# Optimization experiments

Measured on AMD Instinct MI355X. Metric: run time of the kernel, lower is better.

## Reference

```python
import jax, jax.numpy as jnp
import numpy as np


def setup_inputs() -> dict:
    key = jax.random.key(0)
    k1, k2, k3 = jax.random.split(key, 3)
    N, C, H, W, S = 9, 32, 192, 256, 9  # 1 ref + 8 src views, 3x3 patch samples
    f = jax.random.normal(k1, (N, C, H, W, S), dtype=jnp.float32)
    Wp = jax.random.normal(k2, (C, C), dtype=jnp.float32) / np.sqrt(C)  # Conv1d(C,C,1) weight
    bp = jax.random.normal(k3, (C,), dtype=jnp.float32) * 0.01  # Conv1d bias
    return {"f": f, "Wp": Wp, "bp": bp, "o": 2, "G": 8}


def reference(f, Wp, bp, o, G):
    # f: (N, C, H, W, S); view 0 is the reference image, views 1..N-1 are sources.
    N, C, H, W, S = f.shape
    ref = f[0]          # (C, H, W, S)
    src = f[1:]         # (N-1, C, H, W, S)

    # 1x1 Conv1d projection of the reference patches (per-position linear).
    proj = jnp.einsum('dc,chws->dhws', Wp, ref) + bp[:, None, None, None]  # (C,H,W,S)

    # Dot-product attention of the center sample (S//2) against all S samples.
    logits = jnp.sum(proj[:, :, :, S // 2, None] * proj, axis=0) / jnp.sqrt(jnp.float32(C))  # (H,W,S)
    att = jax.nn.softmax(logits, axis=-1)  # (H,W,S)

    # Grouped correlation: split channels into G groups of Cg, dot within each group.
    Cg = C // G
    ref_g = ref.reshape(G, Cg, H, W, S)
    src_g = src.reshape(N - 1, G, Cg, H, W, S)
    gc = jnp.einsum('gchws,ngchws->nghws', ref_g, src_g)  # (N-1, G, H, W, S)

    # Attention-weighted reduction over the S patch-sample axis.
    return jnp.sum(gc * att[None, None], axis=-1)  # (N-1, G, H, W)
```

## Files before the change

### kernel.cpp

```cpp
#include <hip/hip_runtime.h>
#include <math.h>

#define NSRC 8
#define CCH  32
#define HH   192
#define WW   256
#define SS   9
#define GG   8

#define F_SC (HH*WW*SS)
#define F_SH (WW*SS)
#define F_SN (CCH*HH*WW*SS)

#define WS_M   0
#define WS_V   1024
#define WS_BB  1056

__global__ void k0_precompute(const float* __restrict__ Wp,
                              const float* __restrict__ bp,
                              float* __restrict__ ws) {
    const float inv_sqrtC = 0.17677669529663687f;
    int t = threadIdx.x;
    for (int idx = t; idx < 1024; idx += 256) {
        int c = idx >> 5, c2 = idx & 31;
        float acc = 0.f;
        for (int d = 0; d < 32; ++d) acc = fmaf(Wp[d*32 + c], Wp[d*32 + c2], acc);
        ws[WS_M + idx] = acc * inv_sqrtC;
    }
    if (t < 32) {
        float acc = 0.f;
        for (int d = 0; d < 32; ++d) acc = fmaf(Wp[d*32 + t], bp[d], acc);
        ws[WS_V + t] = acc * inv_sqrtC;
    }
    if (t == 0) {
        float acc = 0.f;
        for (int d = 0; d < 32; ++d) acc = fmaf(bp[d], bp[d], acc);
        ws[WS_BB] = acc * inv_sqrtC;
    }
}

__global__ __launch_bounds__(256) void k_fused(const float* __restrict__ f,
                                               const float* __restrict__ ws,
                                               float* __restrict__ out) {
    __shared__ float ref_s[CCH * SS][32];
    __shared__ float M_s[1024];
    __shared__ float v_s[32];
    __shared__ float bb_s;
    __shared__ float lgp[32][8][SS];
    __shared__ float pbeta[32][8];
    __shared__ float att_s[32][SS];

    const int t  = threadIdx.x;
    const int wi = t & 31;
    const int n  = t >> 5;
    const int w  = blockIdx.x * 32 + wi;
    const int h  = blockIdx.y;
    const long base = (long)h * F_SH + (long)w * SS;

    ((float4*)M_s)[t] = ((const float4*)(ws + WS_M))[t];
    if (t < 32) v_s[t] = ws[WS_V + t];
    if (t == 0) bb_s = ws[WS_BB];

    float rref[4 * SS];
    const float* refp = f + base;
    #pragma unroll
    for (int cc = 0; cc < 4; ++cc) {
        const int c = 4 * n + cc;
        const float* rr = refp + (long)c * F_SC;
        #pragma unroll
        for (int s = 0; s < SS; ++s) {
            float v = rr[s];
            rref[cc * SS + s] = v;
            ref_s[c * SS + s][wi] = v;
        }
    }
    __syncthreads();

    float pb = 0.f;
    #pragma unroll
    for (int cc = 0; cc < 4; ++cc)
        pb = fmaf(rref[cc * SS + 4], v_s[4 * n + cc], pb);
    pbeta[wi][n] = pb;

    float u[4];
    #pragma unroll
    for (int cc = 0; cc < 4; ++cc) u[cc] = v_s[4 * n + cc];
    for (int cp = 0; cp < 32; ++cp) {
        float r4 = ref_s[cp * SS + 4][wi];
        #pragma unroll
        for (int cc = 0; cc < 4; ++cc)
            u[cc] = fmaf(M_s[(4 * n + cc) * 32 + cp], r4, u[cc]);
    }

    float lgv[SS];
    #pragma unroll
    for (int s = 0; s < SS; ++s) lgv[s] = 0.f;
    #pragma unroll
    for (int cc = 0; cc < 4; ++cc) {
        float uc = u[cc];
        #pragma unroll
        for (int s = 0; s < SS; ++s)
            lgv[s] = fmaf(uc, rref[cc * SS + s], lgv[s]);
    }
    #pragma unroll
    for (int s = 0; s < SS; ++s) lgp[wi][n][s] = lgv[s];
    __syncthreads();

    if (n == 0) {
        float lt[SS];
        float beta = bb_s;
        #pragma unroll
        for (int nn = 0; nn < 8; ++nn) beta += pbeta[wi][nn];
        #pragma unroll
        for (int s = 0; s < SS; ++s) lt[s] = beta;
        #pragma unroll
        for (int nn = 0; nn < 8; ++nn)
            #pragma unroll
            for (int s = 0; s < SS; ++s) lt[s] += lgp[wi][nn][s];

        float m = lt[0];
        #pragma unroll
        for (int s = 1; s < SS; ++s) m = fmaxf(m, lt[s]);
        float e[SS], sum = 0.f;
        #pragma unroll
        for (int s = 0; s < SS; ++s) { e[s] = __expf(lt[s] - m); sum += e[s]; }
        float inv = 1.f / sum;
        #pragma unroll
        for (int s = 0; s < SS; ++s) att_s[wi][s] = e[s] * inv;
    }
    __syncthreads();

    float a[SS];
    #pragma unroll
    for (int s = 0; s < SS; ++s) a[s] = att_s[wi][s];

    const float* srcp = f + (long)(n + 1) * F_SN + base;

    float acc[GG];
    #pragma unroll
    for (int g = 0; g < GG; ++g) {
        float ps[SS];
        #pragma unroll
        for (int s = 0; s < SS; ++s) ps[s] = 0.f;
        #pragma unroll
        for (int cc = 0; cc < 4; ++cc) {
            const int c = g * 4 + cc;
            const float* sr = srcp + (long)c * F_SC;
            #pragma unroll
            for (int s = 0; s < SS; ++s) {
                float rv = ref_s[c * SS + s][wi];
                ps[s] = fmaf(rv, sr[s], ps[s]);
            }
        }
        float ag = 0.f;
        #pragma unroll
        for (int s = 0; s < SS; ++s) ag = fmaf(a[s], ps[s], ag);
        acc[g] = ag;
    }

    #pragma unroll
    for (int g = 0; g < GG; ++g)
        out[(((long)n * GG + g) * HH + h) * WW + w] = acc[g];
}

extern "C" void kernel_launch(void* const* d_in, const int* in_sizes, int n_in,
                              void* d_out, int out_size, void* d_ws, size_t ws_size,
                              hipStream_t stream) {
    const float* f  = (const float*)d_in[0];
    const float* Wp = (const float*)d_in[1];
    const float* bp = (const float*)d_in[2];
    float* out = (float*)d_out;
    float* ws  = (float*)d_ws;

    k0_precompute<<<1, 256, 0, stream>>>(Wp, bp, ws);
    k_fused<<<dim3(WW / 32, HH), 256, 0, stream>>>(f, ws, out);
}
```

Measured before the change: 665.0 us.

## Stage each view's tile into LDS with direct global-to-LDS loads, loop over sources

```diff
diff --git a/kernel.cpp b/kernel.cpp
--- a/kernel.cpp
+++ b/kernel.cpp
@@ -15,6 +15,11 @@
 #define WS_M   0
 #define WS_V   1024
 #define WS_BB  1056
+
+#define TILE_W  32
+#define ROW_F   (TILE_W * SS)
+#define TILE_F  (CCH * ROW_F)
+#define QPT     9
 
 __global__ void k0_precompute(const float* __restrict__ Wp,
                               const float* __restrict__ bp,
@@ -42,82 +47,88 @@
 __global__ __launch_bounds__(256) void k_fused(const float* __restrict__ f,
                                                const float* __restrict__ ws,
                                                float* __restrict__ out) {
-    __shared__ float ref_s[CCH * SS][32];
+    __shared__ float buf[TILE_F];
     __shared__ float M_s[1024];
     __shared__ float v_s[32];
     __shared__ float bb_s;
-    __shared__ float lgp[32][8][SS];
-    __shared__ float pbeta[32][8];
-    __shared__ float att_s[32][SS];
+    __shared__ float lgp[32 * 73];
+    __shared__ float att_s[32 * SS];
 
     const int t  = threadIdx.x;
     const int wi = t & 31;
-    const int n  = t >> 5;
-    const int w  = blockIdx.x * 32 + wi;
+    const int j  = t >> 5;
+    const int wv = t >> 6;
+    const int w0 = blockIdx.x * TILE_W;
     const int h  = blockIdx.y;
-    const long base = (long)h * F_SH + (long)w * SS;
+    const long rowbase = (long)h * F_SH + (long)w0 * SS;
 
     ((float4*)M_s)[t] = ((const float4*)(ws + WS_M))[t];
     if (t < 32) v_s[t] = ws[WS_V + t];
     if (t == 0) bb_s = ws[WS_BB];
 
+    auto stage = [&](const float* fr) {
+        #pragma unroll
+        for (int i = 0; i < QPT; ++i) {
+            int q = i * 256 + t;
+            int c = q / 72;
+            int k = q - c * 72;
+            const float* g = fr + (long)c * F_SC + rowbase + 4 * k;
+            float* l = buf + (i * 1024 + wv * 256);
+            __builtin_amdgcn_global_load_lds(
+                (const __attribute__((address_space(1))) void*)g,
+                (__attribute__((address_space(3))) void*)l,
+                16, 0, 0);
+        }
+    };
+
+    stage(f);
+    __syncthreads();
+
     float rref[4 * SS];
-    const float* refp = f + base;
     #pragma unroll
     for (int cc = 0; cc < 4; ++cc) {
-        const int c = 4 * n + cc;
-        const float* rr = refp + (long)c * F_SC;
+        const int c = 4 * j + cc;
         #pragma unroll
-        for (int s = 0; s < SS; ++s) {
-            float v = rr[s];
-            rref[cc * SS + s] = v;
-            ref_s[c * SS + s][wi] = v;
-        }
+        for (int s = 0; s < SS; ++s)
+            rref[cc * SS + s] = buf[c * ROW_F + wi * SS + s];
     }
-    __syncthreads();
+
+    float u[4];
+    #pragma unroll
+    for (int cc = 0; cc < 4; ++cc) u[cc] = v_s[4 * j + cc];
+    #pragma unroll
+    for (int cp = 0; cp < 32; ++cp) {
+        float r4 = buf[cp * ROW_F + wi * SS + 4];
+        #pragma unroll
+        for (int cc = 0; cc < 4; ++cc)
+            u[cc] = fmaf(M_s[(4 * j + cc) * 32 + cp], r4, u[cc]);
+    }
 
     float pb = 0.f;
     #pragma unroll
-    for (int cc = 0; cc < 4; ++cc)
-        pb = fmaf(rref[cc * SS + 4], v_s[4 * n + cc], pb);
-    pbeta[wi][n] = pb;
-
-    float u[4];
-    #pragma unroll
-    for (int cc = 0; cc < 4; ++cc) u[cc] = v_s[4 * n + cc];
-    for (int cp = 0; cp < 32; ++cp) {
-        float r4 = ref_s[cp * SS + 4][wi];
-        #pragma unroll
-        for (int cc = 0; cc < 4; ++cc)
-            u[cc] = fmaf(M_s[(4 * n + cc) * 32 + cp], r4, u[cc]);
-    }
+    for (int cc = 0; cc < 4; ++cc) pb = fmaf(rref[cc * SS + 4], v_s[4 * j + cc], pb);
 
     float lgv[SS];
     #pragma unroll
-    for (int s = 0; s < SS; ++s) lgv[s] = 0.f;
+    for (int s = 0; s < SS; ++s) lgv[s] = pb;
     #pragma unroll
     for (int cc = 0; cc < 4; ++cc) {
         float uc = u[cc];
         #pragma unroll
-        for (int s = 0; s < SS; ++s)
-            lgv[s] = fmaf(uc, rref[cc * SS + s], lgv[s]);
+        for (int s = 0; s < SS; ++s) lgv[s] = fmaf(uc, rref[cc * SS + s], lgv[s]);
     }
     #pragma unroll
-    for (int s = 0; s < SS; ++s) lgp[wi][n][s] = lgv[s];
+    for (int s = 0; s < SS; ++s) lgp[wi * 73 + j * SS + s] = lgv[s];
     __syncthreads();
 
-    if (n == 0) {
+    if (j == 0) {
         float lt[SS];
-        float beta = bb_s;
         #pragma unroll
-        for (int nn = 0; nn < 8; ++nn) beta += pbeta[wi][nn];
+        for (int s = 0; s < SS; ++s) lt[s] = bb_s;
         #pragma unroll
-        for (int s = 0; s < SS; ++s) lt[s] = beta;
-        #pragma unroll
-        for (int nn = 0; nn < 8; ++nn)
+        for (int jj = 0; jj < 8; ++jj)
             #pragma unroll
-            for (int s = 0; s < SS; ++s) lt[s] += lgp[wi][nn][s];
-
+            for (int s = 0; s < SS; ++s) lt[s] += lgp[wi * 73 + jj * SS + s];
         float m = lt[0];
         #pragma unroll
         for (int s = 1; s < SS; ++s) m = fmaxf(m, lt[s]);
@@ -126,41 +137,38 @@
         for (int s = 0; s < SS; ++s) { e[s] = __expf(lt[s] - m); sum += e[s]; }
         float inv = 1.f / sum;
         #pragma unroll
-        for (int s = 0; s < SS; ++s) att_s[wi][s] = e[s] * inv;
+        for (int s = 0; s < SS; ++s) att_s[wi * SS + s] = e[s] * inv;
     }
+    stage(f + (long)1 * F_SN);
     __syncthreads();
 
     float a[SS];
     #pragma unroll
-    for (int s = 0; s < SS; ++s) a[s] = att_s[wi][s];
+    for (int s = 0; s < SS; ++s) a[s] = att_s[wi * SS + s];
+    float qv[4 * SS];
+    #pragma unroll
+    for (int cc = 0; cc < 4; ++cc)
+        #pragma unroll
+        for (int s = 0; s < SS; ++s)
+            qv[cc * SS + s] = a[s] * rref[cc * SS + s];
 
-    const float* srcp = f + (long)(n + 1) * F_SN + base;
-
-    float acc[GG];
-    #pragma unroll
-    for (int g = 0; g < GG; ++g) {
-        float ps[SS];
-        #pragma unroll
-        for (int s = 0; s < SS; ++s) ps[s] = 0.f;
+    #pragma unroll 1
+    for (int n = 0; n < NSRC; ++n) {
+        float acc = 0.f;
         #pragma unroll
         for (int cc = 0; cc < 4; ++cc) {
-            const int c = g * 4 + cc;
-            const float* sr = srcp + (long)c * F_SC;
+            const int c = 4 * j + cc;
             #pragma unroll
-            for (int s = 0; s < SS; ++s) {
-                float rv = ref_s[c * SS + s][wi];
-                ps[s] = fmaf(rv, sr[s], ps[s]);
-            }
+            for (int s = 0; s < SS; ++s)
+                acc = fmaf(qv[cc * SS + s], buf[c * ROW_F + wi * SS + s], acc);
         }
-        float ag = 0.f;
-        #pragma unroll
-        for (int s = 0; s < SS; ++s) ag = fmaf(a[s], ps[s], ag);
-        acc[g] = ag;
+        out[(((long)n * GG + j) * HH + h) * WW + w0 + wi] = acc;
+        if (n < NSRC - 1) {
+            __syncthreads();
+            stage(f + (long)(n + 2) * F_SN);
+            __syncthreads();
+        }
     }
-
-    #pragma unroll
-    for (int g = 0; g < GG; ++g)
-        out[(((long)n * GG + g) * HH + h) * WW + w] = acc[g];
 }
 
 extern "C" void kernel_launch(void* const* d_in, const int* in_sizes, int n_in,
@@ -173,5 +181,5 @@
     float* ws  = (float*)d_ws;
 
     k0_precompute<<<1, 256, 0, stream>>>(Wp, bp, ws);
-    k_fused<<<dim3(WW / 32, HH), 256, 0, stream>>>(f, ws, out);
+    k_fused<<<dim3(WW / TILE_W, HH), 256, 0, stream>>>(f, ws, out);
 }
```

After: 659.5 us. About the same (-0.8%).
